# Performance work log

Measured on AMD Instinct MI355X. Metric: run time of the kernel, lower is better.

## Reference

```python
import jax, jax.numpy as jnp
import numpy as np

N_NODES = 50000
N_EDGES = 800000
IN_DIM = 128
HID = 128
LATENT = 64
N_LAYERS = 3
N_GRAPHS = 256
BN_EPS = 1e-5


def setup_inputs() -> dict:
    key = jax.random.key(0)
    ks = jax.random.split(key, 12)
    x = jax.random.normal(ks[0], (N_NODES, IN_DIM), dtype=jnp.float32)
    edge_index = jax.random.randint(ks[1], (2, N_EDGES), 0, N_NODES, dtype=jnp.int32)
    batch = jnp.sort(jax.random.randint(ks[2], (N_NODES,), 0, N_GRAPHS, dtype=jnp.int32))
    s = 1.0 / np.sqrt(HID)
    # stacked per-layer SAGEConv params: lin_l (neighbor path, with bias), lin_r (root path)
    Wl = jax.random.uniform(ks[3], (N_LAYERS, HID, HID), jnp.float32, -s, s)
    bl = jax.random.uniform(ks[4], (N_LAYERS, HID), jnp.float32, -s, s)
    Wr = jax.random.uniform(ks[5], (N_LAYERS, HID, HID), jnp.float32, -s, s)
    gamma = jnp.ones((HID,), jnp.float32)
    beta = jnp.zeros((HID,), jnp.float32)
    fcW = jax.random.uniform(ks[6], (HID, LATENT), jnp.float32, -s, s)
    fcb = jax.random.uniform(ks[7], (LATENT,), jnp.float32, -s, s)
    return {"x": x, "edge_index": edge_index, "batch": batch, "Wl": Wl, "bl": bl,
            "Wr": Wr, "gamma": gamma, "beta": beta, "fcW": fcW, "fcb": fcb}


def _sage_conv(x, src, dst, Wl_i, bl_i, Wr_i):
    # mean-aggregate source features into target nodes (PyG SAGEConv, aggr='mean')
    agg = jax.ops.segment_sum(x[src], dst, num_segments=N_NODES)  # [N, D]
    cnt = jax.ops.segment_sum(jnp.ones((src.shape[0],), x.dtype), dst, num_segments=N_NODES)
    mean = agg / jnp.maximum(cnt, 1.0)[:, None]
    return mean @ Wl_i + bl_i + x @ Wr_i


def reference(x, edge_index, batch, Wl, bl, Wr, gamma, beta, fcW, fcb):
    src, dst = edge_index[0], edge_index[1]
    h = x
    for i in range(N_LAYERS):
        h = _sage_conv(h, src, dst, Wl[i], bl[i], Wr[i])
        h = jax.nn.relu(h)  # dropout: identity at inference
    # global_add_pool over graphs
    pooled = jax.ops.segment_sum(h, batch, num_segments=N_GRAPHS)  # [G, HID]
    # BatchNorm1d over the graph dimension (batch statistics)
    mu = pooled.mean(axis=0)
    var = pooled.var(axis=0)
    normed = (pooled - mu) * jax.lax.rsqrt(var + BN_EPS) * gamma + beta
    return normed @ fcW + fcb
```

## Files before the change

kernel.cpp:

```cpp
#include <hip/hip_runtime.h>
#include <cstdint>
#include <cstddef>

constexpr int HID = 128;
constexpr int LATENT = 64;
constexpr int BSHIFT = 7;
constexpr int NBUCK_MAX = 512;
constexpr int EPB = 1024;

typedef __attribute__((ext_vector_type(8))) short short8;
typedef __attribute__((ext_vector_type(4))) float f32x4;

__device__ inline unsigned short f2bf(float f) {
    unsigned u = __float_as_uint(f);
    u += 0x7fff + ((u >> 16) & 1);
    return (unsigned short)(u >> 16);
}
__device__ inline unsigned pack_bf16x2(float lo, float hi) {
    unsigned ulo = __float_as_uint(lo);
    unsigned uhi = __float_as_uint(hi);
    ulo += 0x7fff + ((ulo >> 16) & 1);
    uhi += 0x7fff + ((uhi >> 16) & 1);
    return (ulo >> 16) | (uhi & 0xffff0000u);
}

__global__ __launch_bounds__(256) void stage1_k(const int* __restrict__ dst,
                                                const float* __restrict__ x,
                                                const float* __restrict__ Wl,
                                                const float* __restrict__ Wr,
                                                int* __restrict__ partial,
                                                unsigned* __restrict__ hx2,
                                                unsigned short* __restrict__ WT,
                                                int* __restrict__ row_ptr,
                                                int nE, int nbuck, int ebB, int n2x, int nN) {
    if (blockIdx.x < (unsigned)ebB) {
        if (blockIdx.x == 0 && threadIdx.x == 0) row_ptr[nN] = nE;
        __shared__ int lh[NBUCK_MAX];
        for (int b = threadIdx.x; b < nbuck; b += 256) lh[b] = 0;
        __syncthreads();
        int base = blockIdx.x * EPB;
        int end = min(base + EPB, nE);
        for (int i = base + threadIdx.x; i < end; i += 256)
            atomicAdd(&lh[dst[i] >> BSHIFT], 1);
        __syncthreads();
        int* row = partial + (size_t)blockIdx.x * NBUCK_MAX;
        for (int b = threadIdx.x; b < nbuck; b += 256) row[b] = lh[b];
    } else if (blockIdx.x < (unsigned)(ebB + 384)) {
        int idx = (blockIdx.x - ebB) * 256 + threadIdx.x;
        int l = idx / (128 * 256);
        int rem = idx % (128 * 256);
        int n = rem / 256;
        int k = rem % 256;
        float v = (k < 128) ? Wl[(size_t)l * 128 * 128 + (size_t)k * 128 + n]
                            : Wr[(size_t)l * 128 * 128 + (size_t)(k - 128) * 128 + n];
        WT[idx] = f2bf(v);
    } else {
        int i = (blockIdx.x - ebB - 384) * 256 + threadIdx.x;
        if (i < n2x) {
            float2 v = ((const float2*)x)[i];
            hx2[i] = pack_bf16x2(v.x, v.y);
        }
    }
}

__global__ __launch_bounds__(256) void colscan_k(int* __restrict__ partial,
                                                 int* __restrict__ bucketTotal, int ebB) {
    int b = blockIdx.x;
    int t = threadIdx.x;
    const int CH = (ebB + 255) / 256;
    int vals[8];
    int s = 0;
    #pragma unroll
    for (int c = 0; c < 8; ++c) {
        if (c >= CH) break;
        int k = t * CH + c;
        int v = (k < ebB) ? partial[(size_t)k * NBUCK_MAX + b] : 0;
        vals[c] = v; s += v;
    }
    __shared__ int part[256];
    part[t] = s;
    __syncthreads();
    for (int d = 1; d < 256; d <<= 1) {
        int u = (t >= d) ? part[t - d] : 0;
        __syncthreads();
        if (t >= d) part[t] += u;
        __syncthreads();
    }
    int run = (t == 0) ? 0 : part[t - 1];
    #pragma unroll
    for (int c = 0; c < 8; ++c) {
        if (c >= CH) break;
        int k = t * CH + c;
        if (k < ebB) partial[(size_t)k * NBUCK_MAX + b] = run;
        run += vals[c];
    }
    if (t == 255) bucketTotal[b] = run;
}

__global__ __launch_bounds__(256) void bplace_k(const int* __restrict__ src,
                                                const int* __restrict__ dst,
                                                const int* __restrict__ partial,
                                                const int* __restrict__ bucketTotal,
                                                uint2* __restrict__ staged, int nE, int nbuck) {
    __shared__ int lh[NBUCK_MAX];
    __shared__ int lb[NBUCK_MAX];
    __shared__ int part[256];
    int t = threadIdx.x;
    for (int b = t; b < nbuck; b += 256) lh[b] = 0;
    int v0 = (2 * t < nbuck) ? bucketTotal[2 * t] : 0;
    int v1 = (2 * t + 1 < nbuck) ? bucketTotal[2 * t + 1] : 0;
    part[t] = v0 + v1;
    __syncthreads();
    for (int d = 1; d < 256; d <<= 1) {
        int u = (t >= d) ? part[t - d] : 0;
        __syncthreads();
        if (t >= d) part[t] += u;
        __syncthreads();
    }
    const int* myPre = partial + (size_t)blockIdx.x * NBUCK_MAX;
    int excl = part[t] - v0 - v1;
    if (2 * t < nbuck)     lb[2 * t]     = excl + myPre[2 * t];
    if (2 * t + 1 < nbuck) lb[2 * t + 1] = excl + v0 + myPre[2 * t + 1];
    __syncthreads();
    int base = blockIdx.x * EPB;
    int end = min(base + EPB, nE);
    for (int i = base + t; i < end; i += 256) {
        int d = dst[i];
        int b = d >> BSHIFT;
        int loc = atomicAdd(&lh[b], 1);
        staged[lb[b] + loc] = make_uint2((unsigned)src[i], (unsigned)d);
    }
}

__global__ __launch_bounds__(256) void sort_bucket_k(const uint2* __restrict__ staged,
                                                     const int* __restrict__ bucketTotal,
                                                     int* __restrict__ row_ptr,
                                                     float* __restrict__ inv,
                                                     int* __restrict__ csr_src, int nN, int nbuck) {
    __shared__ int part[256];
    __shared__ int cnt[128];
    __shared__ int rp[128];
    __shared__ int sBeg;
    int g = blockIdx.x;
    int t = threadIdx.x;
    int v0 = (2 * t < nbuck) ? bucketTotal[2 * t] : 0;
    int v1 = (2 * t + 1 < nbuck) ? bucketTotal[2 * t + 1] : 0;
    part[t] = v0 + v1;
    __syncthreads();
    for (int d = 1; d < 256; d <<= 1) {
        int u = (t >= d) ? part[t - d] : 0;
        __syncthreads();
        if (t >= d) part[t] += u;
        __syncthreads();
    }
    if (t == (g >> 1)) {
        int excl = part[t] - v0 - v1;
        sBeg = (g & 1) ? (excl + v0) : excl;
    }
    if (t < 128) cnt[t] = 0;
    __syncthreads();
    int beg = sBeg;
    int end = beg + bucketTotal[g];
    for (int i = beg + t; i < end; i += 256)
        atomicAdd(&cnt[staged[i].y & 127], 1);
    __syncthreads();
    if (t < 128) rp[t] = cnt[t];
    __syncthreads();
    #pragma unroll
    for (int d = 1; d < 128; d <<= 1) {
        int v = 0;
        if (t < 128 && t >= d) v = rp[t - d];
        __syncthreads();
        if (t < 128 && t >= d) rp[t] += v;
        __syncthreads();
    }
    if (t < 128) {
        int c = cnt[t];
        int excl = rp[t] - c;
        int node = (g << BSHIFT) + t;
        if (node < nN) {
            row_ptr[node] = beg + excl;
            inv[node] = 1.0f / fmaxf((float)c, 1.0f);
        }
        cnt[t] = excl;
    }
    __syncthreads();
    for (int i = beg + t; i < end; i += 256) {
        uint2 e = staged[i];
        int pos = atomicAdd(&cnt[e.y & 127], 1);
        csr_src[beg + pos] = (int)e.x;
    }
}

__global__ __launch_bounds__(256) void gather_k(const int* __restrict__ row_ptr,
                                                const int* __restrict__ csr_src,
                                                const float* __restrict__ inv,
                                                const uint4* __restrict__ h4,
                                                uint4* __restrict__ mean4, int nN) {
    int w = blockIdx.x * 4 + (threadIdx.x >> 6);
    if (w >= nN) return;
    int lane = threadIdx.x & 63;
    int quarter = lane >> 4;
    int col = lane & 15;
    int beg = row_ptr[w], end = row_ptr[w + 1];
    float accA[8] = {}, accB[8] = {}, accC[8] = {}, accD[8] = {};
    for (int base = beg; base < end; base += 64) {
        int navail = min(64, end - base);
        int idx = (lane < navail) ? csr_src[base + lane] : 0;
        for (int j = 0; j < navail; j += 16) {
            int e0 = j + quarter;
            int e1 = j + 4 + quarter;
            int e2 = j + 8 + quarter;
            int e3 = j + 12 + quarter;
            int s0 = __shfl(idx, min(e0, navail - 1), 64);
            int s1 = __shfl(idx, min(e1, navail - 1), 64);
            int s2 = __shfl(idx, min(e2, navail - 1), 64);
            int s3 = __shfl(idx, min(e3, navail - 1), 64);
            uint4 u0 = h4[(size_t)s0 * 16 + col];
            uint4 u1 = h4[(size_t)s1 * 16 + col];
            uint4 u2 = h4[(size_t)s2 * 16 + col];
            uint4 u3 = h4[(size_t)s3 * 16 + col];
            if (e0 < navail) {
                accA[0] += __uint_as_float(u0.x << 16); accA[1] += __uint_as_float(u0.x & 0xffff0000u);
                accA[2] += __uint_as_float(u0.y << 16); accA[3] += __uint_as_float(u0.y & 0xffff0000u);
                accA[4] += __uint_as_float(u0.z << 16); accA[5] += __uint_as_float(u0.z & 0xffff0000u);
                accA[6] += __uint_as_float(u0.w << 16); accA[7] += __uint_as_float(u0.w & 0xffff0000u);
            }
            if (e1 < navail) {
                accB[0] += __uint_as_float(u1.x << 16); accB[1] += __uint_as_float(u1.x & 0xffff0000u);
                accB[2] += __uint_as_float(u1.y << 16); accB[3] += __uint_as_float(u1.y & 0xffff0000u);
                accB[4] += __uint_as_float(u1.z << 16); accB[5] += __uint_as_float(u1.z & 0xffff0000u);
                accB[6] += __uint_as_float(u1.w << 16); accB[7] += __uint_as_float(u1.w & 0xffff0000u);
            }
            if (e2 < navail) {
                accC[0] += __uint_as_float(u2.x << 16); accC[1] += __uint_as_float(u2.x & 0xffff0000u);
                accC[2] += __uint_as_float(u2.y << 16); accC[3] += __uint_as_float(u2.y & 0xffff0000u);
                accC[4] += __uint_as_float(u2.z << 16); accC[5] += __uint_as_float(u2.z & 0xffff0000u);
                accC[6] += __uint_as_float(u2.w << 16); accC[7] += __uint_as_float(u2.w & 0xffff0000u);
            }
            if (e3 < navail) {
                accD[0] += __uint_as_float(u3.x << 16); accD[1] += __uint_as_float(u3.x & 0xffff0000u);
                accD[2] += __uint_as_float(u3.y << 16); accD[3] += __uint_as_float(u3.y & 0xffff0000u);
                accD[4] += __uint_as_float(u3.z << 16); accD[5] += __uint_as_float(u3.z & 0xffff0000u);
                accD[6] += __uint_as_float(u3.w << 16); accD[7] += __uint_as_float(u3.w & 0xffff0000u);
            }
        }
    }
    #pragma unroll
    for (int k = 0; k < 8; ++k) {
        float v = (accA[k] + accB[k]) + (accC[k] + accD[k]);
        v += __shfl_xor(v, 16, 64);
        v += __shfl_xor(v, 32, 64);
        accA[k] = v;
    }
    if (quarter == 0) {
        float iv = inv[w];
        uint4 o;
        o.x = pack_bf16x2(accA[0] * iv, accA[1] * iv);
        o.y = pack_bf16x2(accA[2] * iv, accA[3] * iv);
        o.z = pack_bf16x2(accA[4] * iv, accA[5] * iv);
        o.w = pack_bf16x2(accA[6] * iv, accA[7] * iv);
        mean4[(size_t)w * 16 + col] = o;
    }
}

__global__ __launch_bounds__(256) void sage_mfma_k(
    const unsigned short* __restrict__ mean,
    const unsigned short* __restrict__ h,
    const unsigned short* __restrict__ WT,
    const float* __restrict__ bl,
    unsigned short* __restrict__ out, int nN)
{
    __shared__ unsigned short sB[128 * 256];

    {
        int row = threadIdx.x >> 1, half = threadIdx.x & 1;
        const short8* src = (const short8*)(WT + row * 256 + half * 128);
        int sw = (row & 7) << 2;
        #pragma unroll
        for (int j = 0; j < 16; ++j) {
            int unit = half * 16 + j;
            int unit2 = unit ^ sw;
            *(short8*)(sB + row * 256 + unit2 * 8) = src[j];
        }
    }
    __syncthreads();

    const int wave = threadIdx.x >> 6;
    const int lane = threadIdx.x & 63;
    const int m = lane & 15;
    const int q = lane >> 4;
    const int row = blockIdx.x * 64 + wave * 16 + m;
    const int rowc = min(row, nN - 1);
    const int swm = (m & 7) << 2;

    f32x4 acc[8] = {};
    #pragma unroll
    for (int ks = 0; ks < 8; ++ks) {
        const unsigned short* Aptr = (ks < 4) ? mean : h;
        short8 a = *(const short8*)(Aptr + (size_t)rowc * HID + (ks & 3) * 32 + q * 8);
        #pragma unroll
        for (int t = 0; t < 8; ++t) {
            int unit2 = (ks * 4 + q) ^ swm;
            short8 b = *(const short8*)(sB + (t * 16 + m) * 256 + unit2 * 8);
            acc[t] = __builtin_amdgcn_mfma_f32_16x16x32_bf16(a, b, acc[t], 0, 0, 0);
        }
    }

    int orow_base = blockIdx.x * 64 + wave * 16 + q * 4;
    #pragma unroll
    for (int t = 0; t < 8; ++t) {
        float bias = bl[t * 16 + m];
        #pragma unroll
        for (int r = 0; r < 4; ++r) {
            int orow = orow_base + r;
            if (orow < nN) {
                float v = fmaxf(acc[t][r] + bias, 0.f);
                out[(size_t)orow * HID + t * 16 + m] = f2bf(v);
            }
        }
    }
}

__global__ __launch_bounds__(256) void pool_seg_k(const unsigned* __restrict__ h2,
                                                  const int* __restrict__ batch,
                                                  float* __restrict__ pooled, int nN) {
    int g = blockIdx.x;
    int lo = 0, hi = nN;
    while (lo < hi) { int mid = (lo + hi) >> 1; if (batch[mid] < g) lo = mid + 1; else hi = mid; }
    int beg = lo;
    hi = nN;
    while (lo < hi) { int mid = (lo + hi) >> 1; if (batch[mid] <= g) lo = mid + 1; else hi = mid; }
    int end = lo;

    int lane = threadIdx.x & 63;
    int sub  = threadIdx.x >> 6;
    float s0 = 0.f, s1 = 0.f;
    for (int i = beg + sub; i < end; i += 4) {
        unsigned u = h2[(size_t)i * 64 + lane];
        s0 += __uint_as_float(u << 16);
        s1 += __uint_as_float(u & 0xffff0000u);
    }
    __shared__ float red[4][HID];
    red[sub][2 * lane]     = s0;
    red[sub][2 * lane + 1] = s1;
    __syncthreads();
    if (sub == 0) {
        float v0 = red[0][2 * lane] + red[1][2 * lane] + red[2][2 * lane] + red[3][2 * lane];
        float v1 = red[0][2 * lane + 1] + red[1][2 * lane + 1] + red[2][2 * lane + 1] + red[3][2 * lane + 1];
        pooled[(size_t)g * HID + 2 * lane]     = v0;
        pooled[(size_t)g * HID + 2 * lane + 1] = v1;
    }
}

__global__ __launch_bounds__(1024) void bn_stats_k(const float* __restrict__ pooled,
                                                   const float* __restrict__ gamma,
                                                   const float* __restrict__ beta,
                                                   float* __restrict__ scale,
                                                   float* __restrict__ shift, int nG) {
    __shared__ float rs[8][HID], rs2[8][HID];
    int j = threadIdx.x & (HID - 1);
    int stripe = threadIdx.x >> 7;
    float s = 0.f, s2 = 0.f;
    for (int g = stripe; g < nG; g += 8) {
        float v = pooled[(size_t)g * HID + j];
        s += v; s2 += v * v;
    }
    rs[stripe][j] = s; rs2[stripe][j] = s2;
    __syncthreads();
    if (threadIdx.x < HID) {
        float S = 0.f, S2 = 0.f;
        #pragma unroll
        for (int k = 0; k < 8; ++k) { S += rs[k][j]; S2 += rs2[k][j]; }
        float invG = 1.0f / (float)nG;
        float mu = S * invG;
        float var = S2 * invG - mu * mu;
        float r = rsqrtf(var + 1e-5f) * gamma[j];
        scale[j] = r;
        shift[j] = beta[j] - mu * r;
    }
}

__global__ __launch_bounds__(LATENT) void fc_k(const float* __restrict__ pooled,
                                               const float* __restrict__ scale,
                                               const float* __restrict__ shift,
                                               const float* __restrict__ fcW,
                                               const float* __restrict__ fcb,
                                               float* __restrict__ out, int nG) {
    int g = blockIdx.x;
    int o = threadIdx.x;
    float acc = fcb[o];
    for (int j = 0; j < HID; ++j) {
        float v = pooled[(size_t)g * HID + j] * scale[j] + shift[j];
        acc += v * fcW[(size_t)j * LATENT + o];
    }
    out[(size_t)g * LATENT + o] = acc;
}

extern "C" void kernel_launch(void* const* d_in, const int* in_sizes, int n_in,
                              void* d_out, int out_size, void* d_ws, size_t ws_size,
                              hipStream_t stream) {
    const float* x     = (const float*)d_in[0];
    const int*   ei    = (const int*)d_in[1];
    const int*   batch = (const int*)d_in[2];
    const float* Wl    = (const float*)d_in[3];
    const float* bl    = (const float*)d_in[4];
    const float* Wr    = (const float*)d_in[5];
    const float* gamma = (const float*)d_in[6];
    const float* beta  = (const float*)d_in[7];
    const float* fcW   = (const float*)d_in[8];
    const float* fcb   = (const float*)d_in[9];
    float* out = (float*)d_out;

    const int nN = in_sizes[0] / HID;
    const int nE = in_sizes[1] / 2;
    const int nG = out_size / LATENT;
    const int* src = ei;
    const int* dst = ei + nE;
    const int nbuck = (nN + 127) >> BSHIFT;
    const int ebB = (nE + EPB - 1) / EPB;

    unsigned short* hx   = (unsigned short*)d_ws;
    unsigned short* B1   = hx + (size_t)nN * HID;
    unsigned short* B2   = B1 + (size_t)nN * HID;
    unsigned short* mean = B2 + (size_t)nN * HID;
    unsigned short* WT   = mean + (size_t)nN * HID;
    float* inv    = (float*)(WT + 3 * 128 * 256);
    float* pooled = inv + nN;
    float* scale  = pooled + (size_t)nG * HID;
    float* shift  = scale + HID;
    int*   row_ptr     = (int*)(shift + HID);
    int*   csr_src     = row_ptr + (nN + 1);
    int*   bucketStart = csr_src + nE;
    int*   bucketTotal = bucketStart + NBUCK_MAX + 1;
    int*   partial     = bucketTotal + NBUCK_MAX;
    uint2* staged      = (uint2*)mean;

    const int n2x = nN * HID / 2;
    const int convx_blocks = (n2x + 255) / 256;

    stage1_k<<<ebB + 384 + convx_blocks, 256, 0, stream>>>(dst, x, Wl, Wr, partial,
                                                           (unsigned*)hx, WT, row_ptr,
                                                           nE, nbuck, ebB, n2x, nN);
    colscan_k<<<nbuck, 256, 0, stream>>>(partial, bucketTotal, ebB);
    bplace_k<<<ebB, 256, 0, stream>>>(src, dst, partial, bucketTotal, staged, nE, nbuck);
    sort_bucket_k<<<nbuck, 256, 0, stream>>>(staged, bucketTotal, row_ptr, inv, csr_src, nN, nbuck);

    const int gather_blocks = (nN + 3) / 4;
    const int gemm_blocks = (nN + 63) / 64;

    const unsigned short* hcur = hx;
    unsigned short* outs[3] = {B1, B2, B1};
    for (int l = 0; l < 3; ++l) {
        gather_k<<<gather_blocks, 256, 0, stream>>>(row_ptr, csr_src, inv,
                                                    (const uint4*)hcur, (uint4*)mean, nN);
        sage_mfma_k<<<gemm_blocks, 256, 0, stream>>>(mean, hcur,
                                                     WT + (size_t)l * 128 * 256,
                                                     bl + (size_t)l * HID,
                                                     outs[l], nN);
        hcur = outs[l];
    }

    pool_seg_k<<<nG, 256, 0, stream>>>((const unsigned*)hcur, batch, pooled, nN);
    bn_stats_k<<<1, 1024, 0, stream>>>(pooled, gamma, beta, scale, shift, nG);
    fc_k<<<nG, LATENT, 0, stream>>>(pooled, scale, shift, fcW, fcb, out, nG);
}
```

Before: 316.3 us.

## Fuse CSR build and tail into cooperative kernels with grid sync

Merges the four CSR-construction kernels (histogram, column scan, bucket placement, bucket sort) into one cooperative kernel separated by grid.sync, and does the same for pool, batchnorm stats and FC. Each tail block recomputes the BN statistics redundantly after the grid sync. The GEMM also moves to 512-thread blocks covering 128 rows, so each LDS weight load serves more rows. The aim is to cut kernel-launch and inter-kernel gaps, at the cost of grid-wide barriers and co-residency requirements (ebB blocks of about 782 must all fit at once), with a fallback to the old path if the cooperative launch fails.

```diff
diff --git a/kernel.cpp b/kernel.cpp
--- a/kernel.cpp
+++ b/kernel.cpp
@@ -1,6 +1,9 @@
 #include <hip/hip_runtime.h>
+#include <hip/hip_cooperative_groups.h>
 #include <cstdint>
 #include <cstddef>
+
+namespace cg = cooperative_groups;
 
 constexpr int HID = 128;
 constexpr int LATENT = 64;
@@ -22,6 +25,172 @@
     ulo += 0x7fff + ((ulo >> 16) & 1);
     uhi += 0x7fff + ((uhi >> 16) & 1);
     return (ulo >> 16) | (uhi & 0xffff0000u);
+}
+
+__global__ __launch_bounds__(256) void csr_coop_k(const int* __restrict__ src,
+                                                  const int* __restrict__ dst,
+                                                  const float* __restrict__ x,
+                                                  const float* __restrict__ Wl,
+                                                  const float* __restrict__ Wr,
+                                                  int* __restrict__ partial,
+                                                  unsigned* __restrict__ hx2,
+                                                  unsigned short* __restrict__ WT,
+                                                  int* __restrict__ row_ptr,
+                                                  int* __restrict__ bucketTotal,
+                                                  uint2* __restrict__ staged,
+                                                  float* __restrict__ inv,
+                                                  int* __restrict__ csr_src,
+                                                  int nE, int nN, int nbuck, int ebB, int n2x) {
+    cg::grid_group grid = cg::this_grid();
+    __shared__ int lh[NBUCK_MAX];
+    __shared__ int lb[NBUCK_MAX];
+    __shared__ int part[256];
+    __shared__ int cnt[128];
+    __shared__ int rp[128];
+    __shared__ int sBeg;
+    const int t = threadIdx.x;
+    const int b = blockIdx.x;
+    const int gstride = gridDim.x * 256;
+    const int gtid = b * 256 + t;
+
+    if (b == 0 && t == 0) row_ptr[nN] = nE;
+    for (int i = t; i < nbuck; i += 256) lh[i] = 0;
+    __syncthreads();
+    {
+        int base = b * EPB;
+        int end = min(base + EPB, nE);
+        for (int i = base + t; i < end; i += 256)
+            atomicAdd(&lh[dst[i] >> BSHIFT], 1);
+    }
+    __syncthreads();
+    {
+        int* rowp = partial + (size_t)b * NBUCK_MAX;
+        for (int i = t; i < nbuck; i += 256) rowp[i] = lh[i];
+    }
+    if (gtid < 3 * 128 * 256) {
+        int idx = gtid;
+        int l = idx / (128 * 256);
+        int rem = idx % (128 * 256);
+        int n = rem / 256;
+        int k = rem % 256;
+        float v = (k < 128) ? Wl[(size_t)l * 16384 + (size_t)k * 128 + n]
+                            : Wr[(size_t)l * 16384 + (size_t)(k - 128) * 128 + n];
+        WT[idx] = f2bf(v);
+    }
+    for (int i = gtid; i < n2x; i += gstride) {
+        float2 v = ((const float2*)x)[i];
+        hx2[i] = pack_bf16x2(v.x, v.y);
+    }
+    grid.sync();
+
+    if (b < nbuck) {
+        const int CH = (ebB + 255) / 256;
+        int vals[8];
+        int s = 0;
+        #pragma unroll
+        for (int c = 0; c < 8; ++c) {
+            if (c >= CH) break;
+            int k = t * CH + c;
+            int v = (k < ebB) ? partial[(size_t)k * NBUCK_MAX + b] : 0;
+            vals[c] = v; s += v;
+        }
+        part[t] = s;
+        __syncthreads();
+        for (int d = 1; d < 256; d <<= 1) {
+            int u = (t >= d) ? part[t - d] : 0;
+            __syncthreads();
+            if (t >= d) part[t] += u;
+            __syncthreads();
+        }
+        int run = (t == 0) ? 0 : part[t - 1];
+        #pragma unroll
+        for (int c = 0; c < 8; ++c) {
+            if (c >= CH) break;
+            int k = t * CH + c;
+            if (k < ebB) partial[(size_t)k * NBUCK_MAX + b] = run;
+            run += vals[c];
+        }
+        if (t == 255) bucketTotal[b] = run;
+    }
+    grid.sync();
+
+    {
+        for (int i = t; i < nbuck; i += 256) lh[i] = 0;
+        int v0 = (2 * t < nbuck) ? bucketTotal[2 * t] : 0;
+        int v1 = (2 * t + 1 < nbuck) ? bucketTotal[2 * t + 1] : 0;
+        part[t] = v0 + v1;
+        __syncthreads();
+        for (int d = 1; d < 256; d <<= 1) {
+            int u = (t >= d) ? part[t - d] : 0;
+            __syncthreads();
+            if (t >= d) part[t] += u;
+            __syncthreads();
+        }
+        const int* myPre = partial + (size_t)b * NBUCK_MAX;
+        int excl = part[t] - v0 - v1;
+        if (2 * t < nbuck)     lb[2 * t]     = excl + myPre[2 * t];
+        if (2 * t + 1 < nbuck) lb[2 * t + 1] = excl + v0 + myPre[2 * t + 1];
+        __syncthreads();
+        int base = b * EPB;
+        int end = min(base + EPB, nE);
+        for (int i = base + t; i < end; i += 256) {
+            int d = dst[i];
+            int bk = d >> BSHIFT;
+            int loc = atomicAdd(&lh[bk], 1);
+            staged[lb[bk] + loc] = make_uint2((unsigned)src[i], (unsigned)d);
+        }
+    }
+    grid.sync();
+
+    if (b < nbuck) {
+        int v0 = (2 * t < nbuck) ? bucketTotal[2 * t] : 0;
+        int v1 = (2 * t + 1 < nbuck) ? bucketTotal[2 * t + 1] : 0;
+        part[t] = v0 + v1;
+        __syncthreads();
+        for (int d = 1; d < 256; d <<= 1) {
+            int u = (t >= d) ? part[t - d] : 0;
+            __syncthreads();
+            if (t >= d) part[t] += u;
+            __syncthreads();
+        }
+        if (t == (b >> 1)) {
+            int excl = part[t] - v0 - v1;
+            sBeg = (b & 1) ? (excl + v0) : excl;
+        }
+        if (t < 128) cnt[t] = 0;
+        __syncthreads();
+        int beg = sBeg;
+        int end = beg + bucketTotal[b];
+        for (int i = beg + t; i < end; i += 256)
+            atomicAdd(&cnt[staged[i].y & 127], 1);
+        __syncthreads();
+        if (t < 128) rp[t] = cnt[t];
+        __syncthreads();
+        #pragma unroll
+        for (int d = 1; d < 128; d <<= 1) {
+            int v = 0;
+            if (t < 128 && t >= d) v = rp[t - d];
+            __syncthreads();
+            if (t < 128 && t >= d) rp[t] += v;
+            __syncthreads();
+        }
+        if (t < 128) {
+            int c = cnt[t];
+            int excl = rp[t] - c;
+            int node = (b << BSHIFT) + t;
+            if (node < nN) {
+                row_ptr[node] = beg + excl;
+                inv[node] = 1.0f / fmaxf((float)c, 1.0f);
+            }
+            cnt[t] = excl;
+        }
+        __syncthreads();
+        for (int i = beg + t; i < end; i += 256) {
+            uint2 e = staged[i];
+            int pos = atomicAdd(&cnt[e.y & 127], 1);
+            csr_src[beg + pos] = (int)e.x;
+        }
+    }
 }
 
 __global__ __launch_bounds__(256) void stage1_k(const int* __restrict__ dst,
@@ -51,8 +220,8 @@
         int rem = idx % (128 * 256);
         int n = rem / 256;
         int k = rem % 256;
-        float v = (k < 128) ? Wl[(size_t)l * 128 * 128 + (size_t)k * 128 + n]
-                            : Wr[(size_t)l * 128 * 128 + (size_t)(k - 128) * 128 + n];
+        float v = (k < 128) ? Wl[(size_t)l * 16384 + (size_t)k * 128 + n]
+                            : Wr[(size_t)l * 16384 + (size_t)(k - 128) * 128 + n];
         WT[idx] = f2bf(v);
     } else {
         int i = (blockIdx.x - ebB - 384) * 256 + threadIdx.x;
@@ -264,7 +433,7 @@
     }
 }
 
-__global__ __launch_bounds__(256) void sage_mfma_k(
+__global__ __launch_bounds__(512) void sage_mfma_k(
     const unsigned short* __restrict__ mean,
     const unsigned short* __restrict__ h,
     const unsigned short* __restrict__ WT,
@@ -274,14 +443,14 @@
     __shared__ unsigned short sB[128 * 256];
 
     {
-        int row = threadIdx.x >> 1, half = threadIdx.x & 1;
-        const short8* src = (const short8*)(WT + row * 256 + half * 128);
+        int row = threadIdx.x >> 2, seg = threadIdx.x & 3;
+        const short8* srcp = (const short8*)(WT + row * 256 + seg * 64);
         int sw = (row & 7) << 2;
         #pragma unroll
-        for (int j = 0; j < 16; ++j) {
-            int unit = half * 16 + j;
+        for (int j = 0; j < 8; ++j) {
+            int unit = seg * 8 + j;
             int unit2 = unit ^ sw;
-            *(short8*)(sB + row * 256 + unit2 * 8) = src[j];
+            *(short8*)(sB + row * 256 + unit2 * 8) = srcp[j];
         }
     }
     __syncthreads();
@@ -290,7 +459,7 @@
     const int lane = threadIdx.x & 63;
     const int m = lane & 15;
     const int q = lane >> 4;
-    const int row = blockIdx.x * 64 + wave * 16 + m;
+    const int row = blockIdx.x * 128 + wave * 16 + m;
     const int rowc = min(row, nN - 1);
     const int swm = (m & 7) << 2;
 
@@ -307,7 +476,7 @@
         }
     }
 
-    int orow_base = blockIdx.x * 64 + wave * 16 + q * 4;
+    int orow_base = blockIdx.x * 128 + wave * 16 + q * 4;
     #pragma unroll
     for (int t = 0; t < 8; ++t) {
         float bias = bl[t * 16 + m];
@@ -322,6 +491,89 @@
     }
 }
 
+__global__ __launch_bounds__(256) void tail_coop_k(const unsigned* __restrict__ h2,
+                                                   const int* __restrict__ batch,
+                                                   const float* __restrict__ gamma,
+                                                   const float* __restrict__ beta,
+                                                   const float* __restrict__ fcW,
+                                                   const float* __restrict__ fcb,
+                                                   float* __restrict__ pooled,
+                                                   float* __restrict__ out,
+                                                   int nN, int nG) {
+    cg::grid_group grid = cg::this_grid();
+    const int g = blockIdx.x;
+    const int t = threadIdx.x;
+    __shared__ float red[4][HID];
+    __shared__ float rs[2][HID], rs2[2][HID];
+    __shared__ float scale_s[HID], shift_s[HID];
+    __shared__ float fr[4][LATENT];
+
+    {
+        int lo = 0, hi = nN;
+        while (lo < hi) { int mid = (lo + hi) >> 1; if (batch[mid] < g) lo = mid + 1; else hi = mid; }
+        int beg = lo;
+        hi = nN;
+        while (lo < hi) { int mid = (lo + hi) >> 1; if (batch[mid] <= g) lo = mid + 1; else hi = mid; }
+        int end = lo;
+        int lane = t & 63;
+        int sub = t >> 6;
+        float s0 = 0.f, s1 = 0.f;
+        for (int i = beg + sub; i < end; i += 4) {
+            unsigned u = h2[(size_t)i * 64 + lane];
+            s0 += __uint_as_float(u << 16);
+            s1 += __uint_as_float(u & 0xffff0000u);
+        }
+        red[sub][2 * lane]     = s0;
+        red[sub][2 * lane + 1] = s1;
+        __syncthreads();
+        if (sub == 0) {
+            float v0 = red[0][2 * lane] + red[1][2 * lane] + red[2][2 * lane] + red[3][2 * lane];
+            float v1 = red[0][2 * lane + 1] + red[1][2 * lane + 1] + red[2][2 * lane + 1] + red[3][2 * lane + 1];
+            pooled[(size_t)g * HID + 2 * lane]     = v0;
+            pooled[(size_t)g * HID + 2 * lane + 1] = v1;
+        }
+    }
+    grid.sync();
+
+    {
+        int j = t & (HID - 1);
+        int stripe = t >> 7;
+        float s = 0.f, s2 = 0.f;
+        for (int gg = stripe; gg < nG; gg += 2) {
+            float v = pooled[(size_t)gg * HID + j];
+            s += v; s2 += v * v;
+        }
+        rs[stripe][j] = s; rs2[stripe][j] = s2;
+        __syncthreads();
+        if (t < HID) {
+            float S = rs[0][j] + rs[1][j];
+            float S2 = rs2[0][j] + rs2[1][j];
+            float invG = 1.0f / (float)nG;
+            float mu = S * invG;
+            float var = S2 * invG - mu * mu;
+            float r = rsqrtf(var + 1e-5f) * gamma[j];
+            scale_s[j] = r;
+            shift_s[j] = beta[j] - mu * r;
+        }
+        __syncthreads();
+    }
+
+    {
+        int o = t & 63;
+        int seg = t >> 6;
+        float acc = 0.f;
+        #pragma unroll 8
+        for (int j = seg * 32; j < seg * 32 + 32; ++j) {
+            float v = pooled[(size_t)g * HID + j] * scale_s[j] + shift_s[j];
+            acc += v * fcW[(size_t)j * LATENT + o];
+        }
+        fr[seg][o] = acc;
+        __syncthreads();
+        if (t < LATENT)
+            out[(size_t)g * LATENT + t] = fcb[t] + fr[0][t] + fr[1][t] + fr[2][t] + fr[3][t];
+    }
+}
+
 __global__ __launch_bounds__(256) void pool_seg_k(const unsigned* __restrict__ h2,
                                                   const int* __restrict__ batch,
                                                   float* __restrict__ pooled, int nN) {
@@ -332,7 +584,6 @@
     hi = nN;
     while (lo < hi) { int mid = (lo + hi) >> 1; if (batch[mid] <= g) lo = mid + 1; else hi = mid; }
     int end = lo;
-
     int lane = threadIdx.x & 63;
     int sub  = threadIdx.x >> 6;
     float s0 = 0.f, s1 = 0.f;
@@ -439,29 +690,56 @@
     const int n2x = nN * HID / 2;
     const int convx_blocks = (n2x + 255) / 256;
 
-    stage1_k<<<ebB + 384 + convx_blocks, 256, 0, stream>>>(dst, x, Wl, Wr, partial,
-                                                           (unsigned*)hx, WT, row_ptr,
-                                                           nE, nbuck, ebB, n2x, nN);
-    colscan_k<<<nbuck, 256, 0, stream>>>(partial, bucketTotal, ebB);
-    bplace_k<<<ebB, 256, 0, stream>>>(src, dst, partial, bucketTotal, staged, nE, nbuck);
-    sort_bucket_k<<<nbuck, 256, 0, stream>>>(staged, bucketTotal, row_ptr, inv, csr_src, nN, nbuck);
+    {
+        const int* src_ = src; const int* dst_ = dst;
+        const float* x_ = x; const float* Wl_ = Wl; const float* Wr_ = Wr;
+        int* partial_ = partial; unsigned* hx2_ = (unsigned*)hx; unsigned short* WT_ = WT;
+        int* row_ptr_ = row_ptr; int* bucketTotal_ = bucketTotal;
+        uint2* staged_ = staged; float* inv_ = inv; int* csr_src_ = csr_src;
+        int nE_ = nE, nN_ = nN, nbuck_ = nbuck, ebB_ = ebB, n2x_ = n2x;
+        void* args[] = { &src_, &dst_, &x_, &Wl_, &Wr_, &partial_, &hx2_, &WT_, &row_ptr_,
+                         &bucketTotal_, &staged_, &inv_, &csr_src_,
+                         &nE_, &nN_, &nbuck_, &ebB_, &n2x_ };
+        hipError_t err = hipLaunchCooperativeKernel((void*)csr_coop_k, dim3(ebB), dim3(256),
+                                                    args, 0, stream);
+        if (err != hipSuccess) {
+            stage1_k<<<ebB + 384 + convx_blocks, 256, 0, stream>>>(dst, x, Wl, Wr, partial,
+                                                                   (unsigned*)hx, WT, row_ptr,
+                                                                   nE, nbuck, ebB, n2x, nN);
+            colscan_k<<<nbuck, 256, 0, stream>>>(partial, bucketTotal, ebB);
+            bplace_k<<<ebB, 256, 0, stream>>>(src, dst, partial, bucketTotal, staged, nE, nbuck);
+            sort_bucket_k<<<nbuck, 256, 0, stream>>>(staged, bucketTotal, row_ptr, inv, csr_src, nN, nbuck);
+        }
+    }
 
     const int gather_blocks = (nN + 3) / 4;
-    const int gemm_blocks = (nN + 63) / 64;
+    const int gemm_blocks = (nN + 127) / 128;
 
     const unsigned short* hcur = hx;
     unsigned short* outs[3] = {B1, B2, B1};
     for (int l = 0; l < 3; ++l) {
         gather_k<<<gather_blocks, 256, 0, stream>>>(row_ptr, csr_src, inv,
                                                     (const uint4*)hcur, (uint4*)mean, nN);
-        sage_mfma_k<<<gemm_blocks, 256, 0, stream>>>(mean, hcur,
+        sage_mfma_k<<<gemm_blocks, 512, 0, stream>>>(mean, hcur,
                                                      WT + (size_t)l * 128 * 256,
                                                      bl + (size_t)l * HID,
                                                      outs[l], nN);
         hcur = outs[l];
     }
 
-    pool_seg_k<<<nG, 256, 0, stream>>>((const unsigned*)hcur, batch, pooled, nN);
-    bn_stats_k<<<1, 1024, 0, stream>>>(pooled, gamma, beta, scale, shift, nG);
-    fc_k<<<nG, LATENT, 0, stream>>>(pooled, scale, shift, fcW, fcb, out, nG);
-}
+    {
+        const unsigned* h2_ = (const unsigned*)hcur; const int* batch_ = batch;
+        const float* gamma_ = gamma; const float* beta_ = beta;
+        const float* fcW_ = fcW; const float* fcb_ = fcb;
+        float* pooled_ = pooled; float* out_ = out;
+        int nN_ = nN, nG_ = nG;
+        void* args[] = { &h2_, &batch_, &gamma_, &beta_, &fcW_, &fcb_, &pooled_, &out_, &nN_, &nG_ };
+        hipError_t err = hipLaunchCooperativeKernel((void*)tail_coop_k, dim3(nG), dim3(256),
+                                                    args, 0, stream);
+        if (err != hipSuccess) {
+            pool_seg_k<<<nG, 256, 0, stream>>>((const unsigned*)hcur, batch, pooled, nN);
+            bn_stats_k<<<1, 1024, 0, stream>>>(pooled, gamma, beta, scale, shift, nG);
+            fc_k<<<nG, LATENT, 0, stream>>>(pooled, scale, shift, fcW, fcb, out, nG);
+        }
+    }
+}
```

Measured after the change: 637.9 us. +101.7%, slower.
